# Kernel tuning notes

Measured on AMD Instinct MI355X. Metric: run time of the kernel, lower is better.

The kernel has to match this reference:

```python
import jax, jax.numpy as jnp
import numpy as np

RMIN, RMAX, MAX_PHASE = 0.9, 1.0, 6.283


def setup_inputs() -> dict:
    key = jax.random.key(0)
    ks = jax.random.split(key, 12)
    Bsz, T, U, O, S, H = 16, 4096, 128, 128, 256, 512
    inp = jax.random.normal(ks[0], (Bsz, T, U), dtype=jnp.float32)
    # stable complex diagonal: |lambda| in [RMIN, RMAX], phase in [0, MAX_PHASE]
    r = RMIN + (RMAX - RMIN) * jax.random.uniform(ks[1], (S,), dtype=jnp.float32)
    theta = MAX_PHASE * jax.random.uniform(ks[2], (S,), dtype=jnp.float32)
    Lambda_re = r * jnp.cos(theta)
    Lambda_im = r * jnp.sin(theta)
    B = jax.random.normal(ks[3], (S, U), dtype=jnp.float32) / np.sqrt(U)
    C = jax.random.normal(ks[4], (O, S), dtype=jnp.float32) / np.sqrt(S)
    D = jax.random.normal(ks[5], (O, U), dtype=jnp.float32) / np.sqrt(U)
    W1 = jax.random.normal(ks[6], (H, O), dtype=jnp.float32) / np.sqrt(O)
    W2 = jax.random.normal(ks[7], (H, H), dtype=jnp.float32) / np.sqrt(H)
    W3 = jax.random.normal(ks[8], (O, H), dtype=jnp.float32) / np.sqrt(H)
    Wlin = jax.random.normal(ks[9], (O, U), dtype=jnp.float32) / np.sqrt(U)
    return {"input": inp, "Lambda_re": Lambda_re, "Lambda_im": Lambda_im,
            "B": B, "C": C, "D": D, "W1": W1, "W2": W2, "W3": W3, "Wlin": Wlin}


def _linear_scan(lam, bu):
    # lam: (S,) complex; bu: (B, T, S) complex
    # h_t = lam * h_{t-1} + bu_t, h_0 = 0  (work-efficient associative scan)
    A = jnp.broadcast_to(lam[None, None, :], bu.shape)

    def combine(c1, c2):
        a1, x1 = c1
        a2, x2 = c2
        return a1 * a2, a2 * x1 + x2

    _, h = jax.lax.associative_scan(combine, (A, bu), axis=1)
    return h


def reference(input, Lambda_re, Lambda_im, B, C, D, W1, W2, W3, Wlin):
    lam = (Lambda_re + 1j * Lambda_im).astype(jnp.complex64)        # (S,)
    bu = jnp.einsum('btu,su->bts', input, B).astype(jnp.complex64)   # (B,T,S)
    h = _linear_scan(lam, bu)                                        # (B,T,S) complex
    # LRU readout: real(C h) + D u
    y = jnp.einsum('bts,os->bto', h, C.astype(jnp.complex64)).real \
        + jnp.einsum('btu,ou->bto', input, D)                        # (B,T,O)
    # MLP: Linear->SiLU->Linear->ReLU->Linear (no biases)
    z = jax.nn.silu(y @ W1.T)
    z = jax.nn.relu(z @ W2.T)
    mlp_out = z @ W3.T                                               # (B,T,O)
    # residual linear path
    return mlp_out + input @ Wlin.T
```

## Files before the change

kernel.cpp:

```cpp
#include <hip/hip_runtime.h>
#include <hip/hip_bf16.h>

#define BSZ 16
#define TT 4096
#define UU 128
#define OO 128
#define SS 256
#define HH 512
#define BT (BSZ*TT)
#define CLEN 64
#define NCH (TT/CLEN)

using bf16x8 = __attribute__((ext_vector_type(8))) short;
using f32x4  = __attribute__((ext_vector_type(4))) float;

__device__ __forceinline__ unsigned short f2bf(float x){
  union { float f; unsigned int u; } v; v.f = x;
  unsigned int r = v.u + 0x7fffu + ((v.u >> 16) & 1u);
  return (unsigned short)(r >> 16);
}
__device__ __forceinline__ float bf2f(unsigned short h){
  union { float f; unsigned int u; } v; v.u = ((unsigned int)h) << 16;
  return v.f;
}

#define GLD16(g, s) __builtin_amdgcn_global_load_lds( \
    (const __attribute__((address_space(1))) unsigned int*)(g), \
    (__attribute__((address_space(3))) unsigned int*)(s), 16, 0, 0)

#define SBAR() do{ __builtin_amdgcn_sched_barrier(0); \
                   __builtin_amdgcn_s_barrier(); \
                   __builtin_amdgcn_sched_barrier(0); }while(0)

__global__ __launch_bounds__(256) void split_k(const float* __restrict__ x,
                                               unsigned short* __restrict__ H,
                                               unsigned short* __restrict__ L, int n4){
  int i = blockIdx.x * 256 + threadIdx.x;
  if (i >= n4) return;
  float4 v = ((const float4*)x)[i];
  unsigned short h0 = f2bf(v.x), h1 = f2bf(v.y), h2 = f2bf(v.z), h3 = f2bf(v.w);
  ushort4 hh = make_ushort4(h0, h1, h2, h3);
  ushort4 ll = make_ushort4(f2bf(v.x - bf2f(h0)), f2bf(v.y - bf2f(h1)),
                            f2bf(v.z - bf2f(h2)), f2bf(v.w - bf2f(h3)));
  ((ushort4*)H)[i] = hh;
  ((ushort4*)L)[i] = ll;
}

struct WJobs {
  const float* src[7];
  unsigned short* H[7];
  unsigned short* L[7];
  int end4[7];
};
__global__ __launch_bounds__(256) void split_w(WJobs j, int total4){
  int i = blockIdx.x * 256 + threadIdx.x;
  if (i >= total4) return;
  int t = 0, base = 0;
  #pragma unroll
  for (int k = 0; k < 7; k++){
    if (i >= j.end4[k]){ t = k + 1; base = j.end4[k]; }
  }
  int idx = i - base;
  float4 v = ((const float4*)j.src[t])[idx];
  unsigned short h0 = f2bf(v.x), h1 = f2bf(v.y), h2 = f2bf(v.z), h3 = f2bf(v.w);
  ushort4 hh = make_ushort4(h0, h1, h2, h3);
  ushort4 ll = make_ushort4(f2bf(v.x - bf2f(h0)), f2bf(v.y - bf2f(h1)),
                            f2bf(v.z - bf2f(h2)), f2bf(v.w - bf2f(h3)));
  ((ushort4*)j.H[t])[idx] = hh;
  ((ushort4*)j.L[t])[idx] = ll;
}

__global__ __launch_bounds__(256, 2) void gemm_split(
    const unsigned short* __restrict__ AH1, const unsigned short* __restrict__ AL1,
    const unsigned short* __restrict__ BH1, const unsigned short* __restrict__ BL1, int K1, int f1,
    const unsigned short* __restrict__ AH2, const unsigned short* __restrict__ AL2,
    const unsigned short* __restrict__ BH2, const unsigned short* __restrict__ BL2, int K2, int f2,
    unsigned short* __restrict__ outH, unsigned short* __restrict__ outL,
    float* __restrict__ outF, int Nout, int EPI,
    const float* __restrict__ lre, const float* __restrict__ lim,
    float2* __restrict__ ends)
{
  __shared__ __align__(16) unsigned short SM[32768];
  unsigned short* Ah = SM;
  unsigned short* Al = SM + 8192;
  unsigned short* Bh = SM + 16384;
  unsigned short* Bl = SM + 24576;

  const int tid = threadIdx.x;
  const int mb = blockIdx.x, nb = blockIdx.y;
  const int l = tid & 63, w = tid >> 6;
  const int wr = w >> 1, wc = w & 1;
  const int fr = l & 15, fq = l >> 4;

  f32x4 acc[4][4];
  #pragma unroll
  for (int m = 0; m < 4; m++)
    #pragma unroll
    for (int n = 0; n < 4; n++) acc[m][n] = f32x4{0.f, 0.f, 0.f, 0.f};

  const int nkt = (K1 + K2) >> 5;

  auto STAGE = [&](int buf, int kt){
    const int k0 = kt << 5;
    const unsigned short *aH, *aL, *bH, *bL; int st, kk, flg;
    if (k0 < K1){ aH = AH1; aL = AL1; bH = BH1; bL = BL1; st = K1; kk = k0; flg = f1; }
    else        { aH = AH2; aL = AL2; bH = BH2; bL = BL2; st = K2; kk = k0 - K1; flg = f2; }
    #pragma unroll
    for (int it = 0; it < 2; it++){
      int seg = tid + it * 256;
      int r = seg >> 2, c4 = seg & 3;
      int sc = (c4 ^ ((r >> 1) & 3)) << 3;
      size_t go = (size_t)(mb*128 + r) * st + kk + sc;
      size_t gb = (size_t)(nb*128 + r) * st + kk + sc;
      int lo = buf*4096 + r*32 + c4*8;
      GLD16(aH + go, Ah + lo);
      if (flg & 1) GLD16(aL + go, Al + lo);
      GLD16(bH + gb, Bh + lo);
      if (flg & 2) GLD16(bL + gb, Bl + lo);
    }
  };

  STAGE(0, 0);
  __syncthreads();

  for (int kt = 0; kt < nkt; kt++){
    const int cur = kt & 1;
    const int flg = ((kt << 5) < K1) ? f1 : f2;
    if (kt + 1 < nkt) STAGE(cur ^ 1, kt + 1);

    bf16x8 a_h[4], a_l[4], b_h[4], b_l[4];
    #pragma unroll
    for (int m = 0; m < 4; m++){
      int lra = wr*64 + m*16 + fr;
      int ra = cur*4096 + lra*32 + ((fq ^ ((lra >> 1) & 3)) << 3);
      a_h[m] = *(const bf16x8*)&Ah[ra];
      if (flg & 1) a_l[m] = *(const bf16x8*)&Al[ra];
      int lrb = wc*64 + m*16 + fr;
      int rb = cur*4096 + lrb*32 + ((fq ^ ((lrb >> 1) & 3)) << 3);
      b_h[m] = *(const bf16x8*)&Bh[rb];
      if (flg & 2) b_l[m] = *(const bf16x8*)&Bl[rb];
    }
    __builtin_amdgcn_s_setprio(1);
    #pragma unroll
    for (int m = 0; m < 4; m++)
      #pragma unroll
      for (int n = 0; n < 4; n++)
        acc[m][n] = __builtin_amdgcn_mfma_f32_16x16x32_bf16(a_h[m], b_h[n], acc[m][n], 0, 0, 0);
    if (flg & 1)
      #pragma unroll
      for (int m = 0; m < 4; m++)
        #pragma unroll
        for (int n = 0; n < 4; n++)
          acc[m][n] = __builtin_amdgcn_mfma_f32_16x16x32_bf16(a_l[m], b_h[n], acc[m][n], 0, 0, 0);
    if (flg & 2)
      #pragma unroll
      for (int m = 0; m < 4; m++)
        #pragma unroll
        for (int n = 0; n < 4; n++)
          acc[m][n] = __builtin_amdgcn_mfma_f32_16x16x32_bf16(a_h[m], b_l[n], acc[m][n], 0, 0, 0);
    __builtin_amdgcn_s_setprio(0);

    __syncthreads();
  }

  float* fl = (float*)SM;
  #pragma unroll
  for (int m = 0; m < 4; m++)
    #pragma unroll
    for (int n = 0; n < 4; n++)
      #pragma unroll
      for (int j = 0; j < 4; j++)
        fl[(wr*64 + m*16 + fq*4 + j)*128 + wc*64 + n*16 + fr] = acc[m][n][j];
  __syncthreads();
  #pragma unroll
  for (int it = 0; it < 8; it++){
    int task = tid + (it << 8);
    int rl = task >> 4, cg = task & 15;
    float4 v0 = *(const float4*)&fl[rl*128 + cg*8];
    float4 v1 = *(const float4*)&fl[rl*128 + cg*8 + 4];
    size_t o = (size_t)(mb*128 + rl) * Nout + nb*128 + cg*8;
    if (EPI == 0){
      *(float4*)(outF + o)     = v0;
      *(float4*)(outF + o + 4) = v1;
    } else {
      float xv[8] = {v0.x,v0.y,v0.z,v0.w,v1.x,v1.y,v1.z,v1.w};
      union { unsigned short us[8]; uint4 v; } ph, pl;
      #pragma unroll
      for (int e = 0; e < 8; e++){
        float x = xv[e];
        if (EPI == 2)      x = x / (1.f + __expf(-x));
        else if (EPI == 3) x = fmaxf(x, 0.f);
        ph.us[e] = f2bf(x);
        pl.us[e] = f2bf(x - bf2f(ph.us[e]));
      }
      *(uint4*)(outH + o) = ph.v;
      if (outL) *(uint4*)(outL + o) = pl.v;
    }
  }
  if (ends){
    int c = tid >> 7, sl = tid & 127;
    int b = mb >> 5, chunk = ((mb & 31) << 1) + c;
    int s = nb*128 + sl;
    float lr = lre[s], li = lim[s];
    float hr = 0.f, hi2 = 0.f;
    for (int t = 0; t < 64; t++){
      float x = fl[(c*64 + t)*128 + sl];
      float nr = fmaf(lr, hr, fmaf(-li, hi2, x));
      float ni = fmaf(lr, hi2, li * hr);
      hr = nr; hi2 = ni;
    }
    ends[((size_t)(b*NCH + chunk))*SS + s] = make_float2(hr, hi2);
  }
}

#define ZOFF 0
#define WOFF 65536
#define YOFF (65536 + 2*32768)

__global__ __launch_bounds__(512, 1) void mlp_fused(
    const unsigned short* __restrict__ yH,
    const unsigned short* __restrict__ W1H,
    const unsigned short* __restrict__ W2H,
    unsigned short* __restrict__ z2H)
{
  __shared__ __align__(16) unsigned char LDS[163840];
  const int tid = threadIdx.x;
  const int l = tid & 63, w = tid >> 6;
  const int fr = l & 15, fq = l >> 4;
  const size_t r0 = (size_t)blockIdx.x * 64;

  auto stageW = [&](const unsigned short* W, int Kw, int kt, int slot){
    #pragma unroll
    for (int it = 0; it < 4; it++){
      int seg = tid + (it << 9);
      int r = seg >> 2, c4 = seg & 3;
      GLD16(W + (size_t)r * Kw + kt*32 + ((c4 ^ (r & 3)) << 3),
            LDS + WOFF + slot*32768 + seg*16);
    }
  };

  #pragma unroll
  for (int it = 0; it < 2; it++){
    int seg = tid + (it << 9);
    int r = seg >> 4, c16 = seg & 15;
    GLD16(yH + (size_t)(r0 + r) * UU + ((c16 ^ (r & 7)) << 3),
          LDS + YOFF + seg*16);
  }

  f32x4 acc[4][4];
  #pragma unroll
  for (int m = 0; m < 4; m++)
    #pragma unroll
    for (int n = 0; n < 4; n++) acc[m][n] = f32x4{0.f, 0.f, 0.f, 0.f};

  stageW(W1H, OO, 0, 0);
  stageW(W1H, OO, 1, 1);
  for (int kt = 0; kt < 4; kt++){
    if (kt + 1 < 4) asm volatile("s_waitcnt vmcnt(4)" ::: "memory");
    else            asm volatile("s_waitcnt vmcnt(0)" ::: "memory");
    SBAR();
    const unsigned char* Wb = LDS + WOFF + (kt & 1)*32768;
    bf16x8 a[4], b[4];
    #pragma unroll
    for (int m = 0; m < 4; m++){
      int kc = kt*4 + fq;
      a[m] = *(const bf16x8*)(LDS + YOFF + ((m*16 + fr)*128 + ((kc ^ (fr & 7)) << 3))*2);
    }
    #pragma unroll
    for (int n = 0; n < 4; n++){
      int lrb = w*64 + n*16 + fr;
      b[n] = *(const bf16x8*)(Wb + (lrb*32 + ((fq ^ (lrb & 3)) << 3))*2);
    }
    __builtin_amdgcn_s_setprio(1);
    #pragma unroll
    for (int m = 0; m < 4; m++)
      #pragma unroll
      for (int n = 0; n < 4; n++)
        acc[m][n] = __builtin_amdgcn_mfma_f32_16x16x32_bf16(a[m], b[n], acc[m][n], 0, 0, 0);
    __builtin_amdgcn_s_setprio(0);
    SBAR();
    if (kt + 2 < 4) stageW(W1H, OO, kt + 2, kt & 1);
  }

  unsigned short* Z1 = (unsigned short*)(LDS + ZOFF);
  #pragma unroll
  for (int m = 0; m < 4; m++)
    #pragma unroll
    for (int n = 0; n < 4; n++)
      #pragma unroll
      for (int j = 0; j < 4; j++){
        float x = acc[m][n][j];
        x = x / (1.f + __expf(-x));
        int row = m*16 + fq*4 + j;
        int col = w*64 + n*16 + fr;
        int c64 = col >> 3, ce = col & 7;
        Z1[row*512 + ((c64 ^ (row & 7)) << 3) + ce] = f2bf(x);
      }

  #pragma unroll
  for (int m = 0; m < 4; m++)
    #pragma unroll
    for (int n = 0; n < 4; n++) acc[m][n] = f32x4{0.f, 0.f, 0.f, 0.f};

  stageW(W2H, HH, 0, 0);
  stageW(W2H, HH, 1, 1);
  SBAR();

  for (int kt = 0; kt < 16; kt++){
    if (kt + 2 < 16) stageW(W2H, HH, kt + 2, (kt + 2) % 3);
    if (kt + 2 < 16)      asm volatile("s_waitcnt vmcnt(8)" ::: "memory");
    else if (kt + 1 < 16) asm volatile("s_waitcnt vmcnt(4)" ::: "memory");
    else                  asm volatile("s_waitcnt vmcnt(0)" ::: "memory");
    SBAR();
    const unsigned char* Wb = LDS + WOFF + (kt % 3)*32768;
    bf16x8 a[4], b[4];
    #pragma unroll
    for (int m = 0; m < 4; m++){
      int lra = m*16 + fr;
      int kc = kt*4 + fq;
      a[m] = *(const bf16x8*)(LDS + ZOFF + (lra*512 + ((kc ^ (fr & 7)) << 3))*2);
    }
    #pragma unroll
    for (int n = 0; n < 4; n++){
      int lrb = w*64 + n*16 + fr;
      b[n] = *(const bf16x8*)(Wb + (lrb*32 + ((fq ^ (lrb & 3)) << 3))*2);
    }
    __builtin_amdgcn_s_setprio(1);
    #pragma unroll
    for (int m = 0; m < 4; m++)
      #pragma unroll
      for (int n = 0; n < 4; n++)
        acc[m][n] = __builtin_amdgcn_mfma_f32_16x16x32_bf16(a[m], b[n], acc[m][n], 0, 0, 0);
    __builtin_amdgcn_s_setprio(0);
    SBAR();
  }

  unsigned short* EP = (unsigned short*)(LDS + WOFF);
  #pragma unroll
  for (int m = 0; m < 4; m++)
    #pragma unroll
    for (int n = 0; n < 4; n++)
      #pragma unroll
      for (int j = 0; j < 4; j++){
        float x = fmaxf(acc[m][n][j], 0.f);
        EP[(m*16 + fq*4 + j)*512 + w*64 + n*16 + fr] = f2bf(x);
      }
  __syncthreads();
  #pragma unroll
  for (int it = 0; it < 8; it++){
    int seg = tid + (it << 9);
    int r = seg >> 6, c8 = seg & 63;
    *(uint4*)(z2H + (r0 + r)*HH + c8*8) = *(const uint4*)&EP[r*512 + c8*8];
  }
}

__global__ __launch_bounds__(256) void scan_carries(const float2* __restrict__ ends,
                                                    const float* __restrict__ lre,
                                                    const float* __restrict__ lim,
                                                    float2* __restrict__ carryin){
  const int idx = blockIdx.x * 256 + threadIdx.x;
  const int b = idx >> 8;
  const int s = idx & 255;
  float pr = lre[s], pi = lim[s];
  #pragma unroll
  for (int q = 0; q < 6; q++){
    float nr = pr*pr - pi*pi;
    float ni = 2.f * pr * pi;
    pr = nr; pi = ni;
  }
  float hr = 0.f, hi = 0.f;
  for (int c = 0; c < NCH; c++){
    size_t o = ((size_t)b*NCH + c)*SS + s;
    carryin[o] = make_float2(hr, hi);
    float2 e = ends[o];
    float nr = fmaf(pr, hr, fmaf(-pi, hi, e.x));
    float ni = fmaf(pr, hi, fmaf(pi, hr, e.y));
    hr = nr; hi = ni;
  }
}

__global__ __launch_bounds__(256) void scan_apply_v(
    const unsigned short* __restrict__ buH, const unsigned short* __restrict__ buL,
    const float* __restrict__ lre, const float* __restrict__ lim,
    const float2* __restrict__ carryin, unsigned short* __restrict__ RehH){
  const int tid = threadIdx.x;
  const int grp = tid >> 6, ln = tid & 63;
  const int chunk = blockIdx.x * 4 + grp;
  const int b = chunk >> 6, ch = chunk & 63;
  const int s0 = ln * 4;
  float lr[4], li[4], hr[4], hi[4];
  #pragma unroll
  for (int e = 0; e < 4; e++){ lr[e] = lre[s0+e]; li[e] = lim[s0+e]; }
  const float2* ci = &carryin[((size_t)(b*NCH + ch))*SS + s0];
  #pragma unroll
  for (int e = 0; e < 4; e++){ hr[e] = ci[e].x; hi[e] = ci[e].y; }
  const size_t rbase = ((size_t)b*TT + (size_t)ch*CLEN)*SS + s0;
  for (int t = 0; t < CLEN; t++){
    uint2 hv = *(const uint2*)(buH + rbase + (size_t)t*SS);
    uint2 lv = *(const uint2*)(buL + rbase + (size_t)t*SS);
    const unsigned short* hs = (const unsigned short*)&hv;
    const unsigned short* ls = (const unsigned short*)&lv;
    uint2 ov; unsigned short* os = (unsigned short*)&ov;
    #pragma unroll
    for (int e = 0; e < 4; e++){
      float x = bf2f(hs[e]) + bf2f(ls[e]);
      float nr = fmaf(lr[e], hr[e], fmaf(-li[e], hi[e], x));
      float ni = fmaf(lr[e], hi[e], li[e] * hr[e]);
      hr[e] = nr; hi[e] = ni;
      os[e] = f2bf(nr);
    }
    *(uint2*)(RehH + rbase + (size_t)t*SS) = ov;
  }
}

extern "C" void kernel_launch(void* const* d_in, const int* in_sizes, int n_in,
                              void* d_out, int out_size, void* d_ws, size_t ws_size,
                              hipStream_t stream){
  const float* inp = (const float*)d_in[0];
  const float* lre = (const float*)d_in[1];
  const float* lim = (const float*)d_in[2];
  const float* Bm  = (const float*)d_in[3];
  const float* Cm  = (const float*)d_in[4];
  const float* Dm  = (const float*)d_in[5];
  const float* W1  = (const float*)d_in[6];
  const float* W2  = (const float*)d_in[7];
  const float* W3  = (const float*)d_in[8];
  const float* Wl  = (const float*)d_in[9];
  float* out = (float*)d_out;

  char* ws = (char*)d_ws;
  size_t off = 0;
  auto alloc = [&](size_t bytes)->char*{
    char* p = ws + off; off += (bytes + 255) & ~(size_t)255; return p;
  };
  unsigned short* inH  = (unsigned short*)alloc((size_t)BT*UU*2);
  unsigned short* inL  = (unsigned short*)alloc((size_t)BT*UU*2);
  char* Rbu = alloc((size_t)BT*SS*2*2);
  unsigned short* buH = (unsigned short*)Rbu;
  unsigned short* buL = (unsigned short*)(Rbu + (size_t)BT*SS*2);
  char* R2 = alloc((size_t)BT*HH*2);
  unsigned short* RehH = (unsigned short*)R2;
  unsigned short* yH   = (unsigned short*)(R2 + (size_t)BT*SS*2);
  unsigned short* z2H  = (unsigned short*)Rbu;
  unsigned short* BwH = (unsigned short*)alloc((size_t)SS*UU*2);
  unsigned short* BwL = (unsigned short*)alloc((size_t)SS*UU*2);
  unsigned short* CH_ = (unsigned short*)alloc((size_t)OO*SS*2);
  unsigned short* CL_ = (unsigned short*)alloc((size_t)OO*SS*2);
  unsigned short* DH_ = (unsigned short*)alloc((size_t)OO*UU*2);
  unsigned short* DL_ = (unsigned short*)alloc((size_t)OO*UU*2);
  unsigned short* W1H = (unsigned short*)alloc((size_t)HH*OO*2);
  unsigned short* W1L = (unsigned short*)alloc((size_t)HH*OO*2);
  unsigned short* W2H = (unsigned short*)alloc((size_t)HH*HH*2);
  unsigned short* W2L = (unsigned short*)alloc((size_t)HH*HH*2);
  unsigned short* W3H = (unsigned short*)alloc((size_t)OO*HH*2);
  unsigned short* W3L = (unsigned short*)alloc((size_t)OO*HH*2);
  unsigned short* WlH = (unsigned short*)alloc((size_t)OO*UU*2);
  unsigned short* WlL = (unsigned short*)alloc((size_t)OO*UU*2);
  float2* ends    = (float2*)alloc((size_t)BSZ*NCH*SS*8);
  float2* carryin = (float2*)alloc((size_t)BSZ*NCH*SS*8);
  if (off > ws_size) return;

  split_k<<<(BT*UU/4 + 255)/256, 256, 0, stream>>>(inp, inH, inL, BT*UU/4);
  {
    WJobs j;
    const float* srcs[7] = {Bm, Cm, Dm, W1, W2, W3, Wl};
    unsigned short* Hs[7] = {BwH, CH_, DH_, W1H, W2H, W3H, WlH};
    unsigned short* Ls[7] = {BwL, CL_, DL_, W1L, W2L, W3L, WlL};
    int n4s[7] = {SS*UU/4, OO*SS/4, OO*UU/4, HH*OO/4, HH*HH/4, OO*HH/4, OO*UU/4};
    int cum = 0;
    for (int k = 0; k < 7; k++){
      j.src[k] = srcs[k]; j.H[k] = Hs[k]; j.L[k] = Ls[k];
      cum += n4s[k]; j.end4[k] = cum;
    }
    split_w<<<(cum + 255)/256, 256, 0, stream>>>(j, cum);
  }

  gemm_split<<<dim3(BT/128, SS/128), 256, 0, stream>>>(
      inH, inL, BwH, BwL, UU, 3,
      inH, inL, BwH, BwL, 0,  3,
      buH, buL, nullptr, SS, 1,
      lre, lim, ends);

  scan_carries<<<(BSZ*SS)/256, 256, 0, stream>>>(ends, lre, lim, carryin);

  scan_apply_v<<<BSZ*NCH/4, 256, 0, stream>>>(buH, buL, lre, lim, carryin, RehH);

  gemm_split<<<dim3(BT/128, OO/128), 256, 0, stream>>>(
      RehH, RehH, CH_, CL_, SS, 2,
      inH,  inL,  DH_, DL_, UU, 3,
      yH, nullptr, nullptr, OO, 1,
      nullptr, nullptr, nullptr);

  mlp_fused<<<BT/64, 512, 0, stream>>>(yH, W1H, W2H, z2H);

  gemm_split<<<dim3(BT/128, OO/128), 256, 0, stream>>>(
      z2H, z2H, W3H, W3L, HH, 2,
      inH, inL, WlH, WlL, UU, 3,
      nullptr, nullptr, out, OO, 0,
      nullptr, nullptr, nullptr);
}
```

Measured before the change: 216.5 us.

## Restructure MLP kernel LDS pipeline: bulk-load W1, single barrier per W2 step

The fused MLP kernel now loads all of W1 into LDS in one burst together with the y tile, then runs the first GEMM without per-step barriers or staging. W2 staging uses a three-slot ring that is issued right after the barrier, which drops one barrier per K step. The first two W2 tiles are prefetched before the SiLU epilogue so their loads overlap it. The W2 swizzle changes to (r>>1)&3 to reduce LDS bank conflicts. The risk is the ring-slot reuse safety with a single barrier per step, plus overlapping LDS regions between Z1, the slots and y.

After: 211.6 us. 1.02x faster.

```diff
diff --git a/kernel.cpp b/kernel.cpp
--- a/kernel.cpp
+++ b/kernel.cpp
@@ -213,9 +213,9 @@
   }
 }
 
-#define ZOFF 0
-#define WOFF 65536
-#define YOFF (65536 + 2*32768)
+#define S0OFF 65536
+#define S1OFF 98304
+#define S2OFF 131072
 
 __global__ __launch_bounds__(512, 1) void mlp_fused(
     const unsigned short* __restrict__ yH,
@@ -229,23 +229,31 @@
   const int fr = l & 15, fq = l >> 4;
   const size_t r0 = (size_t)blockIdx.x * 64;
 
-  auto stageW = [&](const unsigned short* W, int Kw, int kt, int slot){
+  auto stageW2 = [&](int kt, int slotoff){
     #pragma unroll
     for (int it = 0; it < 4; it++){
       int seg = tid + (it << 9);
       int r = seg >> 2, c4 = seg & 3;
-      GLD16(W + (size_t)r * Kw + kt*32 + ((c4 ^ (r & 3)) << 3),
-            LDS + WOFF + slot*32768 + seg*16);
+      GLD16(W2H + (size_t)r * HH + kt*32 + ((c4 ^ ((r >> 1) & 3)) << 3),
+            LDS + slotoff + seg*16);
     }
   };
 
+  #pragma unroll
+  for (int it = 0; it < 16; it++){
+    int seg = tid + (it << 9);
+    int r = seg >> 4, c16 = seg & 15;
+    GLD16(W1H + (size_t)r * UU + ((c16 ^ (r & 7)) << 3), LDS + seg*16);
+  }
   #pragma unroll
   for (int it = 0; it < 2; it++){
     int seg = tid + (it << 9);
     int r = seg >> 4, c16 = seg & 15;
     GLD16(yH + (size_t)(r0 + r) * UU + ((c16 ^ (r & 7)) << 3),
-          LDS + YOFF + seg*16);
-  }
+          LDS + S2OFF + seg*16);
+  }
+  asm volatile("s_waitcnt vmcnt(0)" ::: "memory");
+  SBAR();
 
   f32x4 acc[4][4];
   #pragma unroll
@@ -253,23 +261,18 @@
     #pragma unroll
     for (int n = 0; n < 4; n++) acc[m][n] = f32x4{0.f, 0.f, 0.f, 0.f};
 
-  stageW(W1H, OO, 0, 0);
-  stageW(W1H, OO, 1, 1);
+  #pragma unroll
   for (int kt = 0; kt < 4; kt++){
-    if (kt + 1 < 4) asm volatile("s_waitcnt vmcnt(4)" ::: "memory");
-    else            asm volatile("s_waitcnt vmcnt(0)" ::: "memory");
-    SBAR();
-    const unsigned char* Wb = LDS + WOFF + (kt & 1)*32768;
     bf16x8 a[4], b[4];
     #pragma unroll
     for (int m = 0; m < 4; m++){
-      int kc = kt*4 + fq;
-      a[m] = *(const bf16x8*)(LDS + YOFF + ((m*16 + fr)*128 + ((kc ^ (fr & 7)) << 3))*2);
+      int row = m*16 + fr, kc = kt*4 + fq;
+      a[m] = *(const bf16x8*)(LDS + S2OFF + (row*128 + ((kc ^ (row & 7)) << 3))*2);
     }
     #pragma unroll
     for (int n = 0; n < 4; n++){
-      int lrb = w*64 + n*16 + fr;
-      b[n] = *(const bf16x8*)(Wb + (lrb*32 + ((fq ^ (lrb & 3)) << 3))*2);
+      int lrb = w*64 + n*16 + fr, kc = kt*4 + fq;
+      b[n] = *(const bf16x8*)(LDS + (lrb*128 + ((kc ^ (lrb & 7)) << 3))*2);
     }
     __builtin_amdgcn_s_setprio(1);
     #pragma unroll
@@ -278,11 +281,13 @@
       for (int n = 0; n < 4; n++)
         acc[m][n] = __builtin_amdgcn_mfma_f32_16x16x32_bf16(a[m], b[n], acc[m][n], 0, 0, 0);
     __builtin_amdgcn_s_setprio(0);
-    SBAR();
-    if (kt + 2 < 4) stageW(W1H, OO, kt + 2, kt & 1);
-  }
-
-  unsigned short* Z1 = (unsigned short*)(LDS + ZOFF);
+  }
+  SBAR();
+
+  stageW2(0, S0OFF);
+  stageW2(1, S1OFF);
+
+  unsigned short* Z1 = (unsigned short*)LDS;
   #pragma unroll
   for (int m = 0; m < 4; m++)
     #pragma unroll
@@ -296,34 +301,33 @@
         int c64 = col >> 3, ce = col & 7;
         Z1[row*512 + ((c64 ^ (row & 7)) << 3) + ce] = f2bf(x);
       }
+  SBAR();
 
   #pragma unroll
   for (int m = 0; m < 4; m++)
     #pragma unroll
     for (int n = 0; n < 4; n++) acc[m][n] = f32x4{0.f, 0.f, 0.f, 0.f};
 
-  stageW(W2H, HH, 0, 0);
-  stageW(W2H, HH, 1, 1);
-  SBAR();
-
   for (int kt = 0; kt < 16; kt++){
-    if (kt + 2 < 16) stageW(W2H, HH, kt + 2, (kt + 2) % 3);
-    if (kt + 2 < 16)      asm volatile("s_waitcnt vmcnt(8)" ::: "memory");
-    else if (kt + 1 < 16) asm volatile("s_waitcnt vmcnt(4)" ::: "memory");
-    else                  asm volatile("s_waitcnt vmcnt(0)" ::: "memory");
+    if (kt < 15) asm volatile("s_waitcnt vmcnt(4)" ::: "memory");
+    else         asm volatile("s_waitcnt vmcnt(0)" ::: "memory");
     SBAR();
-    const unsigned char* Wb = LDS + WOFF + (kt % 3)*32768;
+    if (kt + 2 < 16){
+      int so = (kt + 2) % 3;
+      stageW2(kt + 2, so == 0 ? S0OFF : (so == 1 ? S1OFF : S2OFF));
+    }
+    const int cs = kt % 3;
+    const unsigned char* Wb = LDS + (cs == 0 ? S0OFF : (cs == 1 ? S1OFF : S2OFF));
     bf16x8 a[4], b[4];
     #pragma unroll
     for (int m = 0; m < 4; m++){
-      int lra = m*16 + fr;
-      int kc = kt*4 + fq;
-      a[m] = *(const bf16x8*)(LDS + ZOFF + (lra*512 + ((kc ^ (fr & 7)) << 3))*2);
+      int row = m*16 + fr, kc = kt*4 + fq;
+      a[m] = *(const bf16x8*)(LDS + (row*512 + ((kc ^ (row & 7)) << 3))*2);
     }
     #pragma unroll
     for (int n = 0; n < 4; n++){
       int lrb = w*64 + n*16 + fr;
-      b[n] = *(const bf16x8*)(Wb + (lrb*32 + ((fq ^ (lrb & 3)) << 3))*2);
+      b[n] = *(const bf16x8*)(Wb + (lrb*32 + ((fq ^ ((lrb >> 1) & 3)) << 3))*2);
     }
     __builtin_amdgcn_s_setprio(1);
     #pragma unroll
@@ -332,10 +336,10 @@
       for (int n = 0; n < 4; n++)
         acc[m][n] = __builtin_amdgcn_mfma_f32_16x16x32_bf16(a[m], b[n], acc[m][n], 0, 0, 0);
     __builtin_amdgcn_s_setprio(0);
-    SBAR();
-  }
-
-  unsigned short* EP = (unsigned short*)(LDS + WOFF);
+  }
+  SBAR();
+
+  unsigned short* EP = (unsigned short*)(LDS + S0OFF);
   #pragma unroll
   for (int m = 0; m < 4; m++)
     #pragma unroll
```
